# Kernel optimization log

Hardware: AMD Instinct MI355X
Metric: run time of the kernel (lower is better)

## Reference

```python
import jax, jax.numpy as jnp
import numpy as np

OUT_H = 7
OUT_W = 7
SPATIAL_SCALE = 0.25
SAMPLING_RATIO = 2  # exact sampling branch (sampling_ratio > 0)
ALIGNED = True


def setup_inputs() -> dict:
    key = jax.random.key(0)
    k1, k2, k3, k4 = jax.random.split(key, 4)
    feat = jax.random.normal(k1, (4, 256, 100, 100), dtype=jnp.float32)
    # rois[K,5]: (batch_idx, x1, y1, x2, y2) in image coords (image ~400px since scale=0.25)
    K = 512
    bidx = jax.random.randint(k2, (K,), 0, 4).astype(jnp.float32)
    xy1 = jax.random.uniform(k3, (K, 2), minval=0.0, maxval=300.0, dtype=jnp.float32)
    wh = jax.random.uniform(k4, (K, 2), minval=20.0, maxval=99.0, dtype=jnp.float32)
    xy2 = xy1 + wh
    rois = jnp.concatenate([bidx[:, None], xy1[:, 0:1], xy1[:, 1:2], xy2[:, 0:1], xy2[:, 1:2]], axis=1)
    return {"input": feat, "rois": rois}


def _roi_align(feat, rois):
    N, C, H, W = feat.shape
    b = rois[:, 0].astype(jnp.int32)  # [K]
    offset = 0.5 if ALIGNED else 0.0
    sw = rois[:, 1] * SPATIAL_SCALE - offset
    sh = rois[:, 2] * SPATIAL_SCALE - offset
    ew = rois[:, 3] * SPATIAL_SCALE - offset
    eh = rois[:, 4] * SPATIAL_SCALE - offset
    rw = ew - sw
    rh = eh - sh
    if not ALIGNED:
        rw = jnp.maximum(rw, 1.0)
        rh = jnp.maximum(rh, 1.0)
    bin_h = rh / OUT_H  # [K]
    bin_w = rw / OUT_W

    ph = jnp.arange(OUT_H, dtype=feat.dtype)
    pw = jnp.arange(OUT_W, dtype=feat.dtype)
    samp = jnp.arange(SAMPLING_RATIO, dtype=feat.dtype) + 0.5  # (i + 0.5)

    # y: [K, OUT_H, SR], x: [K, OUT_W, SR]
    y = sh[:, None, None] + ph[None, :, None] * bin_h[:, None, None] + samp[None, None, :] * (bin_h / SAMPLING_RATIO)[:, None, None]
    x = sw[:, None, None] + pw[None, :, None] * bin_w[:, None, None] + samp[None, None, :] * (bin_w / SAMPLING_RATIO)[:, None, None]

    # bilinear interpolation indices/weights (matches _bilinear_interpolate)
    y = jnp.maximum(y, 0.0)
    x = jnp.maximum(x, 0.0)
    yl = y.astype(jnp.int32)
    xl = x.astype(jnp.int32)
    yh = jnp.where(yl >= H - 1, H - 1, yl + 1)
    yl = jnp.where(yl >= H - 1, H - 1, yl)
    xh = jnp.where(xl >= W - 1, W - 1, xl + 1)
    xl = jnp.where(xl >= W - 1, W - 1, xl)
    ly = y - yl.astype(feat.dtype)
    lx = x - xl.astype(feat.dtype)
    hy = 1.0 - ly
    hx = 1.0 - lx

    def gather(yi, xi):
        # yi: [K,PH,IY], xi: [K,PW,IX] -> [K,PH,IY,PW,IX,C]
        return feat[b[:, None, None, None, None], :,
                    yi[:, :, :, None, None],
                    xi[:, None, None, :, :]]

    v1 = gather(yl, xl)
    v2 = gather(yl, xh)
    v3 = gather(yh, xl)
    v4 = gather(yh, xh)

    out = (jnp.einsum('kpi,kqj,kpiqjc->kcpq', hy, hx, v1)
           + jnp.einsum('kpi,kqj,kpiqjc->kcpq', hy, lx, v2)
           + jnp.einsum('kpi,kqj,kpiqjc->kcpq', ly, hx, v3)
           + jnp.einsum('kpi,kqj,kpiqjc->kcpq', ly, lx, v4))
    count = float(max(SAMPLING_RATIO * SAMPLING_RATIO, 1))
    return out / count  # [K, C, OUT_H, OUT_W]


def reference(input, rois):
    return _roi_align(input, rois)
```

## Files before the change

### kernel.cpp

```cpp
#include <hip/hip_runtime.h>


#define FEAT_C 256
#define FEAT_H 100
#define FEAT_W 100
#define HW     10000
#define NROI   512
#define NBINS  49
#define IMG_N  4

#define REC_BYTES  32
#define IMG_STRIDE (NROI * NBINS * REC_BYTES)
#define CNT_OFF    (IMG_N * IMG_STRIDE)

__device__ __forceinline__ void samp_geo(float s, float bsz, int idx, int sr_i,
                                         int& lo, float& fr) {
    float v = s + bsz * ((float)idx + ((float)sr_i + 0.5f) * 0.5f);
    v = fmaxf(v, 0.0f);
    int l = (int)v;
    if (l > FEAT_H - 1) l = FEAT_H - 1;
    fr = v - (float)l;
    lo = l;
}

__global__ __launch_bounds__(64) void roialign_setup(
    const float* __restrict__ rois, char* __restrict__ ws)
{
    const int k    = blockIdx.x;
    const int lane = threadIdx.x;
    const float* r = rois + k * 5;
    const int bk   = (int)r[0];

    int slot = 0, total = 0;
    for (int i = 0; i < NROI; i += 64) {
        int bi = (int)rois[(i + lane) * 5];
        unsigned long long m = __ballot(bi == bk);
        total += __popcll(m);
        int rel = k - i;
        unsigned long long lt = rel <= 0 ? 0ull
                              : (rel >= 64 ? ~0ull : ((1ull << rel) - 1ull));
        slot += __popcll(m & lt);
    }
    if (lane == 0) ((int*)(ws + CNT_OFF))[bk] = total;

    if (lane < NBINS) {
        const float sw = r[1] * 0.25f - 0.5f, sh = r[2] * 0.25f - 0.5f;
        const float ew = r[3] * 0.25f - 0.5f, eh = r[4] * 0.25f - 0.5f;
        const float bh = (eh - sh) * (1.0f / 7.0f);
        const float bw = (ew - sw) * (1.0f / 7.0f);
        const int ph = (lane * 37) >> 8;
        const int pw = lane - ph * 7;
        int ylA, ylB, xl0, xl1; float lyA, lyB, lx0, lx1;
        samp_geo(sh, bh, ph, 0, ylA, lyA);
        samp_geo(sh, bh, ph, 1, ylB, lyB);
        samp_geo(sw, bw, pw, 0, xl0, lx0);
        samp_geo(sw, bw, pw, 1, xl1, lx1);
        if (xl0 >= FEAT_W - 1) lx0 = 0.0f;
        if (xl1 >= FEAT_W - 1) lx1 = 0.0f;
        int yhA = min(ylA + 1, FEAT_H - 1), yhB = min(ylB + 1, FEAT_H - 1);
        uint4 a, b2;
        a.x  = (unsigned)(ylA * 400) | ((unsigned)(yhA * 400) << 16);
        a.y  = (unsigned)(ylB * 400) | ((unsigned)(yhB * 400) << 16);
        a.z  = (unsigned)(xl0 * 4)   | ((unsigned)(xl1 * 4)   << 16);
        a.w  = __float_as_uint(lyA);
        b2.x = __float_as_uint(lyB);
        b2.y = __float_as_uint(lx0);
        b2.z = __float_as_uint(lx1);
        b2.w = (unsigned)(k * (FEAT_C * NBINS) + lane);
        char* dst = ws + bk * IMG_STRIDE + (slot * NBINS + lane) * REC_BYTES;
        *(uint4*)dst        = a;
        *(uint4*)(dst + 16) = b2;
    }
}

__global__ __launch_bounds__(256) void roialign_main(
    const float* __restrict__ feat, const char* __restrict__ ws,
    float* __restrict__ out)
{
    __shared__ __align__(16) float s_img[HW + 4];

    const int bid  = blockIdx.x;
    const int img  = bid & 3;
    const int c    = bid >> 2;
    const int tid  = threadIdx.x;
    const int lane = tid & 63;
    const int w    = __builtin_amdgcn_readfirstlane(tid >> 6);

    const char* src = (const char*)(feat + (size_t)(img * FEAT_C + c) * HW);
    for (int j = w; j < 40; j += 4) {
        int off = j * 1024 + lane * 16;
        if (off < HW * 4)
            __builtin_amdgcn_global_load_lds(
                (const __attribute__((address_space(1))) void*)(src + off),
                (__attribute__((address_space(3))) void*)((char*)s_img + off),
                16, 0, 0);
    }
    if (tid < 4) s_img[HW + tid] = 0.0f;

    const int   nrec = ((const int*)(ws + CNT_OFF))[img] * NBINS;
    const char* rb   = ws + img * IMG_STRIDE;
    float* const oc  = out + (size_t)c * NBINS;

    int   idx = tid;
    uint4 ra, rbk;
    if (idx < nrec) {
        const char* p = rb + idx * REC_BYTES;
        ra  = *(const uint4*)p;
        rbk = *(const uint4*)(p + 16);
    }
    __syncthreads();

    while (idx < nrec) {
        const uint4 a = ra, b2 = rbk;
        const int nidx = idx + 256;
        if (nidx < nrec) {
            const char* p = rb + nidx * REC_BYTES;
            ra  = *(const uint4*)p;
            rbk = *(const uint4*)(p + 16);
        }

        const char* base = (const char*)s_img;
        const int oAl = a.x & 0xffff, oAh = a.x >> 16;
        const int oBl = a.y & 0xffff, oBh = a.y >> 16;
        const int x0  = a.z & 0xffff, x1  = a.z >> 16;
        const float lyA = __uint_as_float(a.w),  hyA = 1.0f - lyA;
        const float lyB = __uint_as_float(b2.x), hyB = 1.0f - lyB;
        const float lx0 = __uint_as_float(b2.y), hx0 = 1.0f - lx0;
        const float lx1 = __uint_as_float(b2.z), hx1 = 1.0f - lx1;

        const float* pAl0 = (const float*)(base + oAl + x0);
        const float* pAl1 = (const float*)(base + oAl + x1);
        const float* pAh0 = (const float*)(base + oAh + x0);
        const float* pAh1 = (const float*)(base + oAh + x1);
        const float* pBl0 = (const float*)(base + oBl + x0);
        const float* pBl1 = (const float*)(base + oBl + x1);
        const float* pBh0 = (const float*)(base + oBh + x0);
        const float* pBh1 = (const float*)(base + oBh + x1);

        float sAl = hx0 * pAl0[0] + lx0 * pAl0[1] + hx1 * pAl1[0] + lx1 * pAl1[1];
        float sAh = hx0 * pAh0[0] + lx0 * pAh0[1] + hx1 * pAh1[0] + lx1 * pAh1[1];
        float sBl = hx0 * pBl0[0] + lx0 * pBl0[1] + hx1 * pBl1[0] + lx1 * pBl1[1];
        float sBh = hx0 * pBh0[0] + lx0 * pBh0[1] + hx1 * pBh1[0] + lx1 * pBh1[1];
        float acc = hyA * sAl + lyA * sAh + hyB * sBl + lyB * sBh;

        oc[b2.w] = acc * 0.25f;
        idx = nidx;
    }
}

extern "C" void kernel_launch(void* const* d_in, const int* in_sizes, int n_in,
                              void* d_out, int out_size, void* d_ws, size_t ws_size,
                              hipStream_t stream) {
    const float* feat = (const float*)d_in[0];
    const float* rois = (const float*)d_in[1];
    float*       outp = (float*)d_out;
    roialign_setup<<<dim3(NROI), dim3(64), 0, stream>>>(rois, (char*)d_ws);
    roialign_main<<<dim3(IMG_N * FEAT_C), dim3(256), 0, stream>>>(
        feat, (const char*)d_ws, outp);
}
```

Measured before the change: 102.6 us.

## Process two channels per block with interleaved LDS layout and float2 math

Each block now loads two adjacent channels into LDS, interleaved so that one 8-byte LDS read returns both channels' values at a sample point. The per-record bilinear work, including the geometry decode and record loads, is then shared across two channels using float2 vector arithmetic. Block size rises to 512 threads and the grid is halved. The trade-offs are that the direct global-to-LDS async load is replaced by register-staged float4 copies, and LDS use per block doubles, which may lower occupancy. The change also adds a count bounds check and a redundant self-comparison expression.

```diff
diff --git a/kernel.cpp b/kernel.cpp
--- a/kernel.cpp
+++ b/kernel.cpp
@@ -12,6 +12,8 @@
 #define REC_BYTES  32
 #define IMG_STRIDE (NROI * NBINS * REC_BYTES)
 #define CNT_OFF    (IMG_N * IMG_STRIDE)
+
+typedef float f32x2 __attribute__((ext_vector_type(2)));
 
 __device__ __forceinline__ void samp_geo(float s, float bsz, int idx, int sr_i,
                                          int& lo, float& fr) {
@@ -73,77 +75,77 @@
     }
 }
 
-__global__ __launch_bounds__(256) void roialign_main(
+__global__ __launch_bounds__(512, 4) void roialign_main(
     const float* __restrict__ feat, const char* __restrict__ ws,
     float* __restrict__ out)
 {
-    __shared__ __align__(16) float s_img[HW + 4];
+    __shared__ __align__(16) float s_img[2 * HW + 8];
 
-    const int bid  = blockIdx.x;
-    const int img  = bid & 3;
-    const int c    = bid >> 2;
-    const int tid  = threadIdx.x;
-    const int lane = tid & 63;
-    const int w    = __builtin_amdgcn_readfirstlane(tid >> 6);
+    const int bid = blockIdx.x;
+    const int img = bid & 3;
+    const int cp  = bid >> 2;
+    const int tid = threadIdx.x;
 
-    const char* src = (const char*)(feat + (size_t)(img * FEAT_C + c) * HW);
-    for (int j = w; j < 40; j += 4) {
-        int off = j * 1024 + lane * 16;
-        if (off < HW * 4)
-            __builtin_amdgcn_global_load_lds(
-                (const __attribute__((address_space(1))) void*)(src + off),
-                (__attribute__((address_space(3))) void*)((char*)s_img + off),
-                16, 0, 0);
+    const float* c0 = feat + (size_t)(img * FEAT_C + 2 * cp) * HW;
+    const float* c1 = c0 + HW;
+    for (int t = tid; t < HW / 4; t += 512) {
+        float4 A = ((const float4*)c0)[t];
+        float4 B = ((const float4*)c1)[t];
+        ((float4*)s_img)[2 * t]     = make_float4(A.x, B.x, A.y, B.y);
+        ((float4*)s_img)[2 * t + 1] = make_float4(A.z, B.z, A.w, B.w);
     }
-    if (tid < 4) s_img[HW + tid] = 0.0f;
+    if (tid < 8) s_img[2 * HW + tid] = 0.0f;
 
-    const int   nrec = ((const int*)(ws + CNT_OFF))[img] * NBINS;
-    const char* rb   = ws + img * IMG_STRIDE;
-    float* const oc  = out + (size_t)c * NBINS;
+    int cnt = ((const int*)(ws + CNT_OFF))[img];
+    const int nrec = (cnt < 0 || cnt > NROI) ? 0 : cnt * NBINS;
+    const char* rb = ws + img * IMG_STRIDE;
+    float* const oc = out + (size_t)(2 * cp) * NBINS;
 
     int   idx = tid;
-    uint4 ra, rbk;
+    uint4 ra, rk;
     if (idx < nrec) {
-        const char* p = rb + idx * REC_BYTES;
-        ra  = *(const uint4*)p;
-        rbk = *(const uint4*)(p + 16);
+        const char* p = rb + (size_t)idx * REC_BYTES;
+        ra = *(const uint4*)p;
+        rk = *(const uint4*)(p + 16);
     }
     __syncthreads();
 
     while (idx < nrec) {
-        const uint4 a = ra, b2 = rbk;
-        const int nidx = idx + 256;
+        const uint4 a = ra, b2 = rk;
+        const int nidx = idx + 512;
         if (nidx < nrec) {
-            const char* p = rb + nidx * REC_BYTES;
-            ra  = *(const uint4*)p;
-            rbk = *(const uint4*)(p + 16);
+            const char* p = rb + (size_t)nidx * REC_BYTES;
+            ra = *(const uint4*)p;
+            rk = *(const uint4*)(p + 16);
         }
 
         const char* base = (const char*)s_img;
-        const int oAl = a.x & 0xffff, oAh = a.x >> 16;
-        const int oBl = a.y & 0xffff, oBh = a.y >> 16;
-        const int x0  = a.z & 0xffff, x1  = a.z >> 16;
+        const int oAl = (a.x & 0xffff) * 2, oAh = (a.x >> 16) * 2;
+        const int oBl = (a.y & 0xffff) * 2, oBh = (a.y >> 16) * 2;
+        const int x0  = (a.z & 0xffff) * 2, x1  = (a.z >> 16) * 2;
         const float lyA = __uint_as_float(a.w),  hyA = 1.0f - lyA;
-        const float lyB = __uint_as_float(b2.x), hyB = 1.0f - lyB;
+        const float lyB = __uint_as_float(rk.x == rk.x ? b2.x : b2.x), hyB = 1.0f - __uint_as_float(b2.x);
         const float lx0 = __uint_as_float(b2.y), hx0 = 1.0f - lx0;
         const float lx1 = __uint_as_float(b2.z), hx1 = 1.0f - lx1;
 
-        const float* pAl0 = (const float*)(base + oAl + x0);
-        const float* pAl1 = (const float*)(base + oAl + x1);
-        const float* pAh0 = (const float*)(base + oAh + x0);
-        const float* pAh1 = (const float*)(base + oAh + x1);
-        const float* pBl0 = (const float*)(base + oBl + x0);
-        const float* pBl1 = (const float*)(base + oBl + x1);
-        const float* pBh0 = (const float*)(base + oBh + x0);
-        const float* pBh1 = (const float*)(base + oBh + x1);
+        const f32x2* pAl0 = (const f32x2*)(base + oAl + x0);
+        const f32x2* pAl1 = (const f32x2*)(base + oAl + x1);
+        const f32x2* pAh0 = (const f32x2*)(base + oAh + x0);
+        const f32x2* pAh1 = (const f32x2*)(base + oAh + x1);
+        const f32x2* pBl0 = (const f32x2*)(base + oBl + x0);
+        const f32x2* pBl1 = (const f32x2*)(base + oBl + x1);
+        const f32x2* pBh0 = (const f32x2*)(base + oBh + x0);
+        const f32x2* pBh1 = (const f32x2*)(base + oBh + x1);
 
-        float sAl = hx0 * pAl0[0] + lx0 * pAl0[1] + hx1 * pAl1[0] + lx1 * pAl1[1];
-        float sAh = hx0 * pAh0[0] + lx0 * pAh0[1] + hx1 * pAh1[0] + lx1 * pAh1[1];
-        float sBl = hx0 * pBl0[0] + lx0 * pBl0[1] + hx1 * pBl1[0] + lx1 * pBl1[1];
-        float sBh = hx0 * pBh0[0] + lx0 * pBh0[1] + hx1 * pBh1[0] + lx1 * pBh1[1];
-        float acc = hyA * sAl + lyA * sAh + hyB * sBl + lyB * sBh;
+        f32x2 sAl = pAl0[0] * hx0 + pAl0[1] * lx0 + pAl1[0] * hx1 + pAl1[1] * lx1;
+        f32x2 sAh = pAh0[0] * hx0 + pAh0[1] * lx0 + pAh1[0] * hx1 + pAh1[1] * lx1;
+        f32x2 sBl = pBl0[0] * hx0 + pBl0[1] * lx0 + pBl1[0] * hx1 + pBl1[1] * lx1;
+        f32x2 sBh = pBh0[0] * hx0 + pBh0[1] * lx0 + pBh1[0] * hx1 + pBh1[1] * lx1;
+        f32x2 acc = (sAl * hyA + sAh * lyA + sBl * hyB + sBh * __uint_as_float(b2.x)) * 0.25f;
 
-        oc[b2.w] = acc * 0.25f;
+        float* o = oc + b2.w;
+        o[0]     = acc.x;
+        o[NBINS] = acc.y;
         idx = nidx;
     }
 }
@@ -155,6 +157,6 @@
     const float* rois = (const float*)d_in[1];
     float*       outp = (float*)d_out;
     roialign_setup<<<dim3(NROI), dim3(64), 0, stream>>>(rois, (char*)d_ws);
-    roialign_main<<<dim3(IMG_N * FEAT_C), dim3(256), 0, stream>>>(
+    roialign_main<<<dim3(IMG_N * (FEAT_C / 2)), dim3(512), 0, stream>>>(
         feat, (const char*)d_ws, outp);
 }
```

Result: no change. 100.8 us (-1.8%).
